# Kernel tuning notes

Hardware: AMD Instinct MI355X
Metric: run time of the kernel (lower is better)

Reference implementation:

```python
import jax, jax.numpy as jnp
import numpy as np

EPS = 1e-5

def mvn(x):
    # instance norm with torch's unbiased variance (ddof=1), eps added to var
    b, c = x.shape[:2]
    flat = x.reshape(b, c, -1)
    mean = flat.mean(axis=2)[:, :, None, None]
    std = jnp.sqrt(flat.var(axis=2, ddof=1) + EPS)[:, :, None, None]
    return (x - mean) / std

def conv1x1(x, w, b):
    # w: [Cout, Cin], b: [Cout], x: [B, Cin, H, W]
    return jnp.einsum('oc,bchw->bohw', w, x) + b[None, :, None, None]

def setup_inputs() -> dict:
    key = jax.random.key(0)
    ks = jax.random.split(key, 20)
    B, C, H, W = 4, 512, 64, 64
    s = 1.0 / np.sqrt(C)  # kaiming-ish scale for stable softmax logits
    inp = {
        'content': jax.random.normal(ks[0], (B, C, H, W), jnp.float32),
        'style':   jax.random.normal(ks[1], (B, C, H, W), jnp.float32),
        'v_w':   jax.random.normal(ks[2], (C, C), jnp.float32) * s,
        'v_b':   jax.random.normal(ks[3], (C,), jnp.float32) * 0.01,
        'vsp_w': jax.random.normal(ks[4], (1, C), jnp.float32) * s,
        'vsp_b': jax.random.normal(ks[5], (1,), jnp.float32) * 0.01,
        'k_w':   jax.random.normal(ks[6], (C, C), jnp.float32) * s,
        'k_b':   jax.random.normal(ks[7], (C,), jnp.float32) * 0.01,
        'qg_w':  jax.random.normal(ks[8], (C, C), jnp.float32) * s,
        'qg_b':  jax.random.normal(ks[9], (C,), jnp.float32) * 0.01,
        'g1_w1': jax.random.normal(ks[10], (C, C), jnp.float32) * s,
        'g1_b1': jax.random.normal(ks[11], (C,), jnp.float32) * 0.01,
        'g1_w2': jax.random.normal(ks[12], (C, C), jnp.float32) * s,
        'g1_b2': jax.random.normal(ks[13], (C,), jnp.float32) * 0.01,
        'g2_w1': jax.random.normal(ks[14], (C, C), jnp.float32) * s,
        'g2_b1': jax.random.normal(ks[15], (C,), jnp.float32) * 0.01,
        'g2_w2': jax.random.normal(ks[16], (C, C), jnp.float32) * s,
        'g2_b2': jax.random.normal(ks[17], (C,), jnp.float32) * 0.01,
    }
    return inp

def reference(content, style, v_w, v_b, vsp_w, vsp_b, k_w, k_b, qg_w, qg_b,
              g1_w1, g1_b1, g1_w2, g1_b2, g2_w1, g2_b1, g2_w2, g2_b2):
    b, c, h_s, w_s = style.shape
    _, _, h_c, w_c = content.shape
    Ls, Lc = h_s * w_s, h_c * w_c

    V = conv1x1(style, v_w, v_b)                                  # [b,c,hs,ws]
    key_pool = conv1x1(mvn(style), vsp_w, vsp_b).reshape(b, 1, Ls)
    style_weights = jax.nn.softmax(key_pool, axis=-1)             # [b,1,Ls]
    # global style vector: V_flat @ weights^T -> [b,c,1]
    gsv = jnp.einsum('bcl,bl->bc', V.reshape(b, c, Ls), style_weights[:, 0, :])
    gsv4 = gsv[:, :, None, None]                                  # [b,c,1,1]

    Q_guide = conv1x1(mvn(content), qg_w, qg_b)                   # [b,c,hc,wc]
    gamma = conv1x1(jax.nn.relu(conv1x1(gsv4, g1_w1, g1_b1)), g1_w2, g1_b2)
    beta  = conv1x1(jax.nn.relu(conv1x1(gsv4, g2_w1, g2_b1)), g2_w2, g2_b2)
    local_guidance = gamma * Q_guide + beta                       # [b,c,hc,wc]

    Q = (Q_guide + local_guidance).reshape(b, c, Lc).transpose(0, 2, 1)  # [b,Lc,c]
    K = conv1x1(style, k_w, k_b).reshape(b, c, Ls)                       # [b,c,Ls]
    vv = V.reshape(b, c, Ls).transpose(0, 2, 1)                          # [b,Ls,c]

    energy = jnp.einsum('bqc,bck->bqk', Q, K)                     # [b,Lc,Ls]
    S = jax.nn.softmax(energy, axis=-1)
    out = jnp.einsum('bqk,bkc->bqc', S, vv)                       # [b,Lc,c]
    out = out.transpose(0, 2, 1).reshape(b, c, h_c, w_c)
    return mvn(content) + out
```

## Files before the change

kernel.cpp:

```cpp
#include <hip/hip_runtime.h>
#include <math.h>

typedef __bf16 bf16_t;
typedef _Float16 f16_t;
typedef __attribute__((ext_vector_type(8))) __bf16 bf16x8;
typedef __attribute__((ext_vector_type(8))) _Float16 f16x8;
typedef __attribute__((ext_vector_type(4))) float f32x4;

namespace {
constexpr int Bn = 4;
constexpr int Cn = 512;
constexpr int Ln = 4096;
constexpr float kEps = 1e-5f;
constexpr size_t NQK = (size_t)Bn * Ln * Cn;
constexpr size_t CC  = (size_t)Cn * Cn;

constexpr size_t FOFF_MEANS = 0;
constexpr size_t FOFF_RSTDS = 2048;
constexpr size_t FOFF_MEANC = 4096;
constexpr size_t FOFF_RSTDC = 6144;
constexpr size_t FOFF_KP    = 8192;
constexpr size_t FOFF_GSV   = FOFF_KP + 16384;
constexpr size_t FOFF_H1    = FOFF_GSV + 2048;
constexpr size_t FOFF_H2    = FOFF_H1 + 2048;
constexpr size_t FOFF_GAMMA = FOFF_H2 + 2048;
constexpr size_t FOFF_BETA  = FOFF_GAMMA + 2048;
}

__device__ inline f32x4 mfma_bf(bf16x8 a, bf16x8 b, f32x4 c) {
    return __builtin_amdgcn_mfma_f32_16x16x32_bf16(a, b, c, 0, 0, 0);
}
__device__ inline f32x4 mfma_f16(f16x8 a, f16x8 b, f32x4 c) {
    return __builtin_amdgcn_mfma_f32_16x16x32_f16(a, b, c, 0, 0, 0);
}

__device__ __forceinline__ void gll16(const void* g, void* l) {
    __builtin_amdgcn_global_load_lds((const unsigned int*)g, (unsigned int*)l, 16, 0, 0);
}

__device__ inline unsigned short h2u(f16_t x) {
    union { f16_t h; unsigned short u; } c; c.h = x; return c.u;
}
__device__ inline f16_t u2h(unsigned short x) {
    union { f16_t h; unsigned short u; } c; c.u = x; return c.h;
}

__global__ __launch_bounds__(256) void stats_kernel(const float* __restrict__ x,
                                                    float* __restrict__ mean,
                                                    float* __restrict__ rstd) {
    int bc = blockIdx.x;
    const float* row = x + (size_t)bc * Ln;
    float s1 = 0.f, s2 = 0.f;
    for (int i = threadIdx.x; i < Ln; i += 256) {
        float v = row[i];
        s1 += v; s2 += v * v;
    }
    for (int off = 32; off; off >>= 1) {
        s1 += __shfl_down(s1, off);
        s2 += __shfl_down(s2, off);
    }
    __shared__ float a1[4], a2[4];
    int wid = threadIdx.x >> 6;
    if ((threadIdx.x & 63) == 0) { a1[wid] = s1; a2[wid] = s2; }
    __syncthreads();
    if (threadIdx.x == 0) {
        s1 = a1[0] + a1[1] + a1[2] + a1[3];
        s2 = a2[0] + a2[1] + a2[2] + a2[3];
        float m = s1 / Ln;
        float var = (s2 - m * s1) / (Ln - 1);
        mean[bc] = m;
        rstd[bc] = 1.0f / sqrtf(var + kEps);
    }
}

__global__ __launch_bounds__(256) void split_w_kernel(const float* __restrict__ w0,
                                                      const float* __restrict__ w1,
                                                      const float* __restrict__ w2,
                                                      bf16_t* __restrict__ wsp) {
    const float* w = (blockIdx.y == 0) ? w0 : (blockIdx.y == 1) ? w1 : w2;
    bf16_t* hi = wsp + (size_t)blockIdx.y * 2 * CC;
    bf16_t* lo = hi + CC;
    size_t i0 = ((size_t)blockIdx.x * 256 + threadIdx.x) * 8;
    float4 a = *(const float4*)(w + i0);
    float4 b = *(const float4*)(w + i0 + 4);
    float vs[8] = {a.x, a.y, a.z, a.w, b.x, b.y, b.z, b.w};
    bf16x8 hv, lv;
#pragma unroll
    for (int i = 0; i < 8; i++) {
        bf16_t h = (bf16_t)vs[i];
        hv[i] = h;
        lv[i] = (bf16_t)(vs[i] - (float)h);
    }
    *(bf16x8*)(hi + i0) = hv;
    *(bf16x8*)(lo + i0) = lv;
}

template <bool MVN>
__global__ __launch_bounds__(256) void split_xt_kernel(const float* __restrict__ x,
                                                       const float* __restrict__ mean,
                                                       const float* __restrict__ rstd,
                                                       bf16_t* __restrict__ hi,
                                                       bf16_t* __restrict__ lo) {
    __shared__ bf16_t th[32][40];
    __shared__ bf16_t tl[32][40];
    int b = blockIdx.z, c0 = blockIdx.y * 32, l0 = blockIdx.x * 32;
    const size_t base = (size_t)b * Cn * Ln;
    int lc = threadIdx.x & 31;
    int cr0 = threadIdx.x >> 5;
#pragma unroll
    for (int p = 0; p < 4; p++) {
        int cr = cr0 + p * 8;
        float v = x[base + (size_t)(c0 + cr) * Ln + l0 + lc];
        if constexpr (MVN) {
            v = (v - mean[b * Cn + c0 + cr]) * rstd[b * Cn + c0 + cr];
        }
        bf16_t h = (bf16_t)v;
        th[lc][cr] = h;
        tl[lc][cr] = (bf16_t)(v - (float)h);
    }
    __syncthreads();
    int tt = threadIdx.x & 127;
    int lrow = tt >> 2;
    int c8 = (tt & 3) * 8;
    if (threadIdx.x < 128) {
        *(bf16x8*)(hi + base + (size_t)(l0 + lrow) * Cn + c0 + c8) = *(bf16x8*)&th[lrow][c8];
    } else {
        *(bf16x8*)(lo + base + (size_t)(l0 + lrow) * Cn + c0 + c8) = *(bf16x8*)&tl[lrow][c8];
    }
}

template <int MODE>
__global__ __launch_bounds__(256, 2) void conv_mfma_kernel(
    const bf16_t* __restrict__ Whi, const bf16_t* __restrict__ Wlo,
    const bf16_t* __restrict__ Xhi, const bf16_t* __restrict__ Xlo,
    const float* __restrict__ bias,
    const float* __restrict__ gma, const float* __restrict__ bta,
    f16_t* __restrict__ out0) {
    const int b = blockIdx.z;
    const int o0 = blockIdx.y * 128;
    const int l0 = blockIdx.x * 128;
    const int tid = threadIdx.x;
    const int lane = tid & 63, wid = tid >> 6;
    const int wm = wid & 1, wn = wid >> 1;
    const int lg = lane >> 4, li = lane & 15;
    const size_t bLC = (size_t)b * Ln * Cn;

    __shared__ __align__(16) char smem[66560];

    f32x4 acc[4][4];
#pragma unroll
    for (int i = 0; i < 4; i++)
#pragma unroll
        for (int j = 0; j < 4; j++) acc[i][j] = (f32x4){0.f, 0.f, 0.f, 0.f};

    for (int cc = 0; cc < Cn; cc += 64) {
        __syncthreads();
#pragma unroll
        for (int p = 0; p < 4; p++) {
            int idx = p * 256 + tid;
            int row = idx >> 3;
            int c8 = (idx & 7) * 8;
            unsigned off = (unsigned)((row * 64 + c8) * 2) ^ (unsigned)((row & 7) << 4);
            *(bf16x8*)(smem + off)         = *(const bf16x8*)(Whi + (size_t)(o0 + row) * Cn + cc + c8);
            *(bf16x8*)(smem + 16384 + off) = *(const bf16x8*)(Wlo + (size_t)(o0 + row) * Cn + cc + c8);
            *(bf16x8*)(smem + 32768 + off) = *(const bf16x8*)(Xhi + bLC + (size_t)(l0 + row) * Cn + cc + c8);
            *(bf16x8*)(smem + 49152 + off) = *(const bf16x8*)(Xlo + bLC + (size_t)(l0 + row) * Cn + cc + c8);
        }
        __syncthreads();
#pragma unroll
        for (int k2 = 0; k2 < 2; k2++) {
            bf16x8 ah[4], al[4], bh[4], bl[4];
#pragma unroll
            for (int f = 0; f < 4; f++) {
                int row = wm * 64 + f * 16 + li;
                unsigned ob = (unsigned)(row * 128 + ((k2 * 64 + lg * 16) ^ ((row & 7) << 4)));
                ah[f] = *(const bf16x8*)(smem + ob);
                al[f] = *(const bf16x8*)(smem + 16384 + ob);
            }
#pragma unroll
            for (int f = 0; f < 4; f++) {
                int row = wn * 64 + f * 16 + li;
                unsigned ob = (unsigned)(row * 128 + ((k2 * 64 + lg * 16) ^ ((row & 7) << 4)));
                bh[f] = *(const bf16x8*)(smem + 32768 + ob);
                bl[f] = *(const bf16x8*)(smem + 49152 + ob);
            }
#pragma unroll
            for (int fm = 0; fm < 4; fm++)
#pragma unroll
                for (int fn = 0; fn < 4; fn++) {
                    acc[fm][fn] = mfma_bf(ah[fm], bh[fn], acc[fm][fn]);
                    acc[fm][fn] = mfma_bf(ah[fm], bl[fn], acc[fm][fn]);
                    acc[fm][fn] = mfma_bf(al[fm], bh[fn], acc[fm][fn]);
                }
        }
    }

    if constexpr (MODE == 0) {
        const size_t bCL = (size_t)b * Cn * Ln;
#pragma unroll
        for (int fm = 0; fm < 4; fm++) {
#pragma unroll
            for (int r = 0; r < 4; r++) {
                int o = o0 + wm * 64 + fm * 16 + lg * 4 + r;
                float bv = bias[o];
#pragma unroll
                for (int fn = 0; fn < 4; fn++) {
                    int l = l0 + wn * 64 + fn * 16 + li;
                    out0[bCL + (size_t)o * Ln + l] = (f16_t)(acc[fm][fn][r] + bv);
                }
            }
        }
    } else {
        __syncthreads();
        unsigned short* ep = (unsigned short*)smem;
#pragma unroll
        for (int fm = 0; fm < 4; fm++) {
#pragma unroll
            for (int r = 0; r < 4; r++) {
                int orow = wm * 64 + fm * 16 + lg * 4 + r;
                int o = o0 + orow;
                float bv = bias[o];
                float gv = 0.f, btv = 0.f;
                if constexpr (MODE == 2) { gv = gma[b * Cn + o]; btv = bta[b * Cn + o]; }
#pragma unroll
                for (int fn = 0; fn < 4; fn++) {
                    int lrow = wn * 64 + fn * 16 + li;
                    float v = acc[fm][fn][r] + bv;
                    if constexpr (MODE == 2) v = v * (1.f + gv) + btv;
                    ep[lrow * 130 + orow] = h2u((f16_t)v);
                }
            }
        }
        __syncthreads();
#pragma unroll
        for (int p = 0; p < 8; p++) {
            int idx = p * 256 + tid;
            int lrow = idx >> 4;
            int c8 = (idx & 15) * 8;
            f16x8 hv;
#pragma unroll
            for (int u = 0; u < 8; u++) hv[u] = u2h(ep[lrow * 130 + c8 + u]);
            *(f16x8*)(out0 + bLC + (size_t)(l0 + lrow) * Cn + o0 + c8) = hv;
        }
    }
}

__global__ __launch_bounds__(256) void keypool_kernel(const float* __restrict__ style,
                                                      const float* __restrict__ vsp_w,
                                                      const float* __restrict__ vsp_b,
                                                      const float* __restrict__ mean_s,
                                                      const float* __restrict__ rstd_s,
                                                      float* __restrict__ kp) {
    int b = blockIdx.y;
    int l = blockIdx.x * 256 + threadIdx.x;
    const size_t bCL = (size_t)b * Cn * Ln;
    float acc = 0.f;
    for (int c = 0; c < Cn; c++) {
        float v = style[bCL + (size_t)c * Ln + l];
        acc += vsp_w[c] * (v - mean_s[b * Cn + c]) * rstd_s[b * Cn + c];
    }
    kp[b * Ln + l] = acc + vsp_b[0];
}

__global__ __launch_bounds__(1024) void softmax_kp_kernel(float* __restrict__ kp) {
    int b = blockIdx.x;
    float* p = kp + (size_t)b * Ln;
    int tid = threadIdx.x;
    float v[4];
    float m = -3e38f;
#pragma unroll
    for (int j = 0; j < 4; j++) { v[j] = p[tid + 1024 * j]; m = fmaxf(m, v[j]); }
    __shared__ float red[16];
    for (int off = 32; off; off >>= 1) m = fmaxf(m, __shfl_down(m, off));
    if ((tid & 63) == 0) red[tid >> 6] = m;
    __syncthreads();
    if (tid == 0) {
        float mm = red[0];
        for (int i = 1; i < 16; i++) mm = fmaxf(mm, red[i]);
        red[0] = mm;
    }
    __syncthreads();
    m = red[0];
    __syncthreads();
    float e[4]; float s = 0.f;
#pragma unroll
    for (int j = 0; j < 4; j++) { e[j] = __expf(v[j] - m); s += e[j]; }
    for (int off = 32; off; off >>= 1) s += __shfl_down(s, off);
    if ((tid & 63) == 0) red[tid >> 6] = s;
    __syncthreads();
    if (tid == 0) {
        float ss = 0.f;
        for (int i = 0; i < 16; i++) ss += red[i];
        red[0] = ss;
    }
    __syncthreads();
    float inv = 1.0f / red[0];
#pragma unroll
    for (int j = 0; j < 4; j++) p[tid + 1024 * j] = e[j] * inv;
}

__global__ __launch_bounds__(256) void gsv_kernel(const f16_t* __restrict__ Vf,
                                                  const float* __restrict__ w,
                                                  float* __restrict__ gsv) {
    int c = blockIdx.x, b = blockIdx.y;
    int tid = threadIdx.x;
    const f16_t* vp = Vf + ((size_t)b * Cn + c) * Ln;
    const float* wp = w + (size_t)b * Ln;
    float acc = 0.f;
    for (int base = tid * 8; base < Ln; base += 2048) {
        f16x8 v = *(const f16x8*)(vp + base);
        float4 w0 = *(const float4*)(wp + base);
        float4 w1 = *(const float4*)(wp + base + 4);
        acc += (float)v[0] * w0.x + (float)v[1] * w0.y + (float)v[2] * w0.z + (float)v[3] * w0.w;
        acc += (float)v[4] * w1.x + (float)v[5] * w1.y + (float)v[6] * w1.z + (float)v[7] * w1.w;
    }
    for (int off = 32; off; off >>= 1) acc += __shfl_down(acc, off);
    __shared__ float red[4];
    if ((tid & 63) == 0) red[tid >> 6] = acc;
    __syncthreads();
    if (tid == 0) gsv[(size_t)b * Cn + c] = red[0] + red[1] + red[2] + red[3];
}

__global__ __launch_bounds__(256) void mlp_hidden_kernel(const float* __restrict__ gsv,
                                                         const float* __restrict__ w1a, const float* __restrict__ b1a,
                                                         const float* __restrict__ w1b, const float* __restrict__ b1b,
                                                         float* __restrict__ h1, float* __restrict__ h2) {
    int idx = blockIdx.x * 256 + threadIdx.x;
    int b = idx / Cn, c = idx % Cn;
    float a1 = b1a[c], a2 = b1b[c];
    for (int k = 0; k < Cn; k++) {
        float g = gsv[b * Cn + k];
        a1 += w1a[(size_t)c * Cn + k] * g;
        a2 += w1b[(size_t)c * Cn + k] * g;
    }
    h1[idx] = fmaxf(a1, 0.f);
    h2[idx] = fmaxf(a2, 0.f);
}

__global__ __launch_bounds__(256) void mlp_out_kernel(const float* __restrict__ h1, const float* __restrict__ h2,
                                                      const float* __restrict__ w2a, const float* __restrict__ b2a,
                                                      const float* __restrict__ w2b, const float* __restrict__ b2b,
                                                      float* __restrict__ gamma, float* __restrict__ beta) {
    int idx = blockIdx.x * 256 + threadIdx.x;
    int b = idx / Cn, c = idx % Cn;
    float a1 = b2a[c], a2 = b2b[c];
    for (int k = 0; k < Cn; k++) {
        a1 += w2a[(size_t)c * Cn + k] * h1[b * Cn + k];
        a2 += w2b[(size_t)c * Cn + k] * h2[b * Cn + k];
    }
    gamma[idx] = a1;
    beta[idx] = a2;
}

__global__ __launch_bounds__(256, 2) void flash_kernel(
    const f16_t* __restrict__ Qf, const f16_t* __restrict__ Kf,
    const f16_t* __restrict__ Vf, float* __restrict__ Ot) {
    const int b = blockIdx.y;
    const int q0 = blockIdx.x * 32;
    const int tid = threadIdx.x;
    const int lane = tid & 63;
    const int wn = tid >> 6;
    const int lg = lane >> 4, li = lane & 15;

    __shared__ __align__(16) f16_t q_s[32 * 512];
    __shared__ __align__(16) f16_t pb_s[32 * 64];
    __shared__ float smx[4][32];
    __shared__ float sml[4][32];

    const size_t qbase = ((size_t)b * Ln + q0) * Cn;
    const size_t kbase = (size_t)b * Ln * Cn;
    const size_t vbase = (size_t)b * Cn * Ln;

#pragma unroll
    for (int i = 0; i < 8; i++) {
        int idx = i * 256 + tid;
        int row = idx >> 6, slot = idx & 63;
        int sp = (slot & 56) | ((slot & 7) ^ (row & 7));
        gll16(Qf + qbase + (size_t)row * Cn + sp * 8, q_s + (size_t)idx * 8);
    }
    __syncthreads();

    const int key = wn * 16 + li;

    f16x8 kreg[2][2];
    auto loadK = [&](int g, int slot) {
        int ktA = (g >> 3) << 6;
        int cc = (g & 7) * 64;
        const f16_t* kp = Kf + kbase + (size_t)(ktA + key) * Cn + cc + lg * 8;
        kreg[slot][0] = *(const f16x8*)(kp);
        kreg[slot][1] = *(const f16x8*)(kp + 32);
    };
    loadK(0, 0);
    loadK(1, 1);

    f32x4 o[2][8];
#pragma unroll
    for (int m = 0; m < 2; m++)
#pragma unroll
        for (int j = 0; j < 8; j++) o[m][j] = (f32x4){0.f, 0.f, 0.f, 0.f};
    float m_run[2][4], l_run[2][4];
#pragma unroll
    for (int m = 0; m < 2; m++)
#pragma unroll
        for (int r = 0; r < 4; r++) { m_run[m][r] = -1e30f; l_run[m][r] = 0.f; }

    for (int tile = 0; tile < 64; tile++) {
        const int kt = tile * 64;
        f32x4 e[2];
#pragma unroll
        for (int m = 0; m < 2; m++) e[m] = (f32x4){0.f, 0.f, 0.f, 0.f};

#pragma unroll
        for (int cs = 0; cs < 8; cs++) {
            const int slot = cs & 1;
            f16x8 k0 = kreg[slot][0], k1 = kreg[slot][1];
            {
                int g2 = (tile * 8 + cs + 2) & 511;
                loadK(g2, slot);
            }
            f16x8 aq0[2], aq1[2];
#pragma unroll
            for (int m = 0; m < 2; m++) {
                int row = m * 16 + li;
                unsigned swz = (unsigned)((row & 7) << 4);
                aq0[m] = *(const f16x8*)((const char*)q_s + row * 1024 + ((cs * 128 + lg * 16) ^ swz));
                aq1[m] = *(const f16x8*)((const char*)q_s + row * 1024 + ((cs * 128 + 64 + lg * 16) ^ swz));
            }
            __builtin_amdgcn_s_setprio(1);
#pragma unroll
            for (int m = 0; m < 2; m++) {
                e[m] = mfma_f16(aq0[m], k0, e[m]);
                e[m] = mfma_f16(aq1[m], k1, e[m]);
            }
            __builtin_amdgcn_s_setprio(0);
        }

        f16x8 va[2], vb[2];
        {
            const f16_t* vp0 = Vf + vbase + (size_t)(wn * 16 + li) * Ln + kt + lg * 8;
            va[0] = *(const f16x8*)(vp0);
            vb[0] = *(const f16x8*)(vp0 + 32);
            const f16_t* vp1 = Vf + vbase + (size_t)((4 + wn) * 16 + li) * Ln + kt + lg * 8;
            va[1] = *(const f16x8*)(vp1);
            vb[1] = *(const f16x8*)(vp1 + 32);
        }

        float tmax[2][4];
#pragma unroll
        for (int m = 0; m < 2; m++)
#pragma unroll
            for (int r = 0; r < 4; r++) tmax[m][r] = e[m][r];
#pragma unroll
        for (int d = 1; d < 16; d <<= 1)
#pragma unroll
            for (int m = 0; m < 2; m++)
#pragma unroll
                for (int r = 0; r < 4; r++) tmax[m][r] = fmaxf(tmax[m][r], __shfl_xor(tmax[m][r], d));
        if (li == 0) {
#pragma unroll
            for (int m = 0; m < 2; m++)
#pragma unroll
                for (int r = 0; r < 4; r++) smx[wn][m * 16 + lg * 4 + r] = tmax[m][r];
        }
        asm volatile("s_waitcnt lgkmcnt(0)\n\ts_barrier" ::: "memory");
        float scv[2][4];
        bool anyresc = false;
#pragma unroll
        for (int m = 0; m < 2; m++)
#pragma unroll
            for (int r = 0; r < 4; r++) {
                int row = m * 16 + lg * 4 + r;
                float tm = fmaxf(fmaxf(smx[0][row], smx[1][row]), fmaxf(smx[2][row], smx[3][row]));
                float mnew = fmaxf(m_run[m][r], tm);
                scv[m][r] = __expf(m_run[m][r] - mnew);
                anyresc |= (mnew > m_run[m][r]);
                m_run[m][r] = mnew;
            }
        float pv[2][4], rsum[2][4];
#pragma unroll
        for (int m = 0; m < 2; m++)
#pragma unroll
            for (int r = 0; r < 4; r++) {
                float pe = __expf(e[m][r] - m_run[m][r]);
                pv[m][r] = pe;
                rsum[m][r] = pe;
            }
#pragma unroll
        for (int d = 1; d < 16; d <<= 1)
#pragma unroll
            for (int m = 0; m < 2; m++)
#pragma unroll
                for (int r = 0; r < 4; r++) rsum[m][r] += __shfl_xor(rsum[m][r], d);
        if (li == 0) {
#pragma unroll
            for (int m = 0; m < 2; m++)
#pragma unroll
                for (int r = 0; r < 4; r++) sml[wn][m * 16 + lg * 4 + r] = rsum[m][r];
        }
#pragma unroll
        for (int m = 0; m < 2; m++)
#pragma unroll
            for (int r = 0; r < 4; r++) {
                int qrow = m * 16 + lg * 4 + r;
                unsigned boff = (unsigned)(qrow * 128 + ((2 * key) ^ ((qrow & 7) << 4)));
                *(f16_t*)((char*)pb_s + boff) = (f16_t)pv[m][r];
            }
        if (__any((int)anyresc)) {
#pragma unroll
            for (int m = 0; m < 2; m++)
#pragma unroll
                for (int j = 0; j < 8; j++)
#pragma unroll
                    for (int r = 0; r < 4; r++) o[m][j][r] *= scv[m][r];
        }
        asm volatile("s_waitcnt lgkmcnt(0)\n\ts_barrier" ::: "memory");
#pragma unroll
        for (int m = 0; m < 2; m++)
#pragma unroll
            for (int r = 0; r < 4; r++) {
                int row = m * 16 + lg * 4 + r;
                l_run[m][r] = l_run[m][r] * scv[m][r] + sml[0][row] + sml[1][row] + sml[2][row] + sml[3][row];
            }

        f16x8 pa[2][2];
#pragma unroll
        for (int m = 0; m < 2; m++)
#pragma unroll
            for (int k2 = 0; k2 < 2; k2++) {
                int qrow = m * 16 + li;
                pa[m][k2] = *(const f16x8*)((const char*)pb_s + qrow * 128 +
                              ((k2 * 64 + lg * 16) ^ ((qrow & 7) << 4)));
            }
#pragma unroll
        for (int n = 0; n < 8; n++) {
            const int slot = n & 1;
            f16x8 c0 = va[slot], c1 = vb[slot];
            if (n + 2 < 8) {
                int cg = (n + 2) * 4 + wn;
                const f16_t* vp = Vf + vbase + (size_t)(cg * 16 + li) * Ln + kt + lg * 8;
                va[slot] = *(const f16x8*)(vp);
                vb[slot] = *(const f16x8*)(vp + 32);
            }
            __builtin_amdgcn_s_setprio(1);
#pragma unroll
            for (int m = 0; m < 2; m++) {
                o[m][n] = mfma_f16(pa[m][0], c0, o[m][n]);
                o[m][n] = mfma_f16(pa[m][1], c1, o[m][n]);
            }
            __builtin_amdgcn_s_setprio(0);
        }
    }

#pragma unroll
    for (int m = 0; m < 2; m++)
#pragma unroll
        for (int r = 0; r < 4; r++) l_run[m][r] = 1.f / l_run[m][r];
#pragma unroll
    for (int m = 0; m < 2; m++)
#pragma unroll
        for (int n = 0; n < 8; n++) {
            int c = (n * 4 + wn) * 16 + li;
            int qg = q0 + m * 16 + lg * 4;
            float4 ov;
            ov.x = o[m][n][0] * l_run[m][0];
            ov.y = o[m][n][1] * l_run[m][1];
            ov.z = o[m][n][2] * l_run[m][2];
            ov.w = o[m][n][3] * l_run[m][3];
            *(float4*)(Ot + vbase + (size_t)c * Ln + qg) = ov;
        }
}

__global__ __launch_bounds__(256) void final_kernel(const float* __restrict__ content,
                                                    const float* __restrict__ mean_c,
                                                    const float* __restrict__ rstd_c,
                                                    float* __restrict__ out) {
    size_t gid = (size_t)blockIdx.x * 256 + threadIdx.x;
    size_t linear = gid * 4;
    int ch = (int)(linear / Ln);
    float m = mean_c[ch], rs = rstd_c[ch];
    float4 cv = *(const float4*)(content + linear);
    float4 ov = *(const float4*)(out + linear);
    ov.x += (cv.x - m) * rs;
    ov.y += (cv.y - m) * rs;
    ov.z += (cv.z - m) * rs;
    ov.w += (cv.w - m) * rs;
    *(float4*)(out + linear) = ov;
}

extern "C" void kernel_launch(void* const* d_in, const int* in_sizes, int n_in,
                              void* d_out, int out_size, void* d_ws, size_t ws_size,
                              hipStream_t stream) {
    const float* content = (const float*)d_in[0];
    const float* style   = (const float*)d_in[1];
    const float* v_w   = (const float*)d_in[2];
    const float* v_b   = (const float*)d_in[3];
    const float* vsp_w = (const float*)d_in[4];
    const float* vsp_b = (const float*)d_in[5];
    const float* k_w   = (const float*)d_in[6];
    const float* k_b   = (const float*)d_in[7];
    const float* qg_w  = (const float*)d_in[8];
    const float* qg_b  = (const float*)d_in[9];
    const float* g1_w1 = (const float*)d_in[10];
    const float* g1_b1 = (const float*)d_in[11];
    const float* g1_w2 = (const float*)d_in[12];
    const float* g1_b2 = (const float*)d_in[13];
    const float* g2_w1 = (const float*)d_in[14];
    const float* g2_b1 = (const float*)d_in[15];
    const float* g2_w2 = (const float*)d_in[16];
    const float* g2_b2 = (const float*)d_in[17];

    f16_t* wsh = (f16_t*)d_ws;
    f16_t* Qf = wsh;
    f16_t* Kf = wsh + NQK;
    f16_t* Vf = wsh + 2 * NQK;
    bf16_t* wsp = (bf16_t*)(wsh + 3 * NQK);
    bf16_t* Wv_hi = wsp;            bf16_t* Wv_lo = wsp + CC;
    bf16_t* Wk_hi = wsp + 2 * CC;   bf16_t* Wk_lo = wsp + 3 * CC;
    bf16_t* Wq_hi = wsp + 4 * CC;   bf16_t* Wq_lo = wsp + 5 * CC;

    float* wsf = (float*)(wsp + 6 * CC);
    float* mean_s = wsf + FOFF_MEANS;
    float* rstd_s = wsf + FOFF_RSTDS;
    float* mean_c = wsf + FOFF_MEANC;
    float* rstd_c = wsf + FOFF_RSTDC;
    float* kp     = wsf + FOFF_KP;
    float* gsv    = wsf + FOFF_GSV;
    float* h1     = wsf + FOFF_H1;
    float* h2     = wsf + FOFF_H2;
    float* gamma  = wsf + FOFF_GAMMA;
    float* beta   = wsf + FOFF_BETA;

    bf16_t* XThi = (bf16_t*)d_out;
    bf16_t* XTlo = XThi + NQK;
    float* outF  = (float*)d_out;

    stats_kernel<<<dim3(Bn * Cn), 256, 0, stream>>>(style, mean_s, rstd_s);
    stats_kernel<<<dim3(Bn * Cn), 256, 0, stream>>>(content, mean_c, rstd_c);

    split_w_kernel<<<dim3(CC / 2048, 3), 256, 0, stream>>>(v_w, k_w, qg_w, wsp);
    split_xt_kernel<false><<<dim3(Ln / 32, Cn / 32, Bn), 256, 0, stream>>>(style, nullptr, nullptr, XThi, XTlo);

    dim3 cgrid(Ln / 128, Cn / 128, Bn);
    conv_mfma_kernel<0><<<cgrid, 256, 0, stream>>>(Wv_hi, Wv_lo, XThi, XTlo, v_b, nullptr, nullptr, Vf);

    keypool_kernel<<<dim3(Ln / 256, Bn), 256, 0, stream>>>(style, vsp_w, vsp_b, mean_s, rstd_s, kp);
    softmax_kp_kernel<<<dim3(Bn), 1024, 0, stream>>>(kp);
    gsv_kernel<<<dim3(Cn, Bn), 256, 0, stream>>>(Vf, kp, gsv);
    mlp_hidden_kernel<<<dim3(Bn * Cn / 256), 256, 0, stream>>>(gsv, g1_w1, g1_b1, g2_w1, g2_b1, h1, h2);
    mlp_out_kernel<<<dim3(Bn * Cn / 256), 256, 0, stream>>>(h1, h2, g1_w2, g1_b2, g2_w2, g2_b2, gamma, beta);

    conv_mfma_kernel<1><<<cgrid, 256, 0, stream>>>(Wk_hi, Wk_lo, XThi, XTlo, k_b, nullptr, nullptr, Kf);

    split_xt_kernel<true><<<dim3(Ln / 32, Cn / 32, Bn), 256, 0, stream>>>(content, mean_c, rstd_c, XThi, XTlo);
    conv_mfma_kernel<2><<<cgrid, 256, 0, stream>>>(Wq_hi, Wq_lo, XThi, XTlo, qg_b, gamma, beta, Qf);

    flash_kernel<<<dim3(Ln / 32, Bn), 256, 0, stream>>>(Qf, Kf, Vf, outF);

    final_kernel<<<dim3((Bn * Cn * (Ln / 4)) / 256), 256, 0, stream>>>(content, mean_c, rstd_c, outF);
}
```

Measured before the change: 709.0 us.

## Halve flash query tile to 16 rows and remap blocks across XCDs

Each flash-attention workgroup now handles 16 query rows instead of 32, doubling the grid to 1024 blocks. A 1D grid with an XCD-aware remap (bid&7)*128+(bid>>3) groups blocks of the same batch on the same chiplet, aiming for better L2 reuse of K/V. The QK accumulation is split into two independent MFMA chains to increase ILP. The trade-off is that K and V are re-read from memory twice as often per query, and fewer MFMAs are issued per load and per barrier.

After: 1.145 ms. 1.61x slower.

```diff
diff --git a/kernel.cpp b/kernel.cpp
--- a/kernel.cpp
+++ b/kernel.cpp
@@ -355,24 +355,27 @@
 __global__ __launch_bounds__(256, 2) void flash_kernel(
     const f16_t* __restrict__ Qf, const f16_t* __restrict__ Kf,
     const f16_t* __restrict__ Vf, float* __restrict__ Ot) {
-    const int b = blockIdx.y;
-    const int q0 = blockIdx.x * 32;
+    const int bid = blockIdx.x;
+    const int wgid = (bid & 7) * 128 + (bid >> 3);
+    const int b = wgid >> 8;
+    const int q0 = (wgid & 255) * 16;
+
     const int tid = threadIdx.x;
     const int lane = tid & 63;
     const int wn = tid >> 6;
     const int lg = lane >> 4, li = lane & 15;
 
-    __shared__ __align__(16) f16_t q_s[32 * 512];
-    __shared__ __align__(16) f16_t pb_s[32 * 64];
-    __shared__ float smx[4][32];
-    __shared__ float sml[4][32];
+    __shared__ __align__(16) f16_t q_s[16 * 512];
+    __shared__ __align__(16) f16_t pb_s[16 * 64];
+    __shared__ float smx[4][16];
+    __shared__ float sml[4][16];
 
     const size_t qbase = ((size_t)b * Ln + q0) * Cn;
     const size_t kbase = (size_t)b * Ln * Cn;
     const size_t vbase = (size_t)b * Cn * Ln;
 
 #pragma unroll
-    for (int i = 0; i < 8; i++) {
+    for (int i = 0; i < 4; i++) {
         int idx = i * 256 + tid;
         int row = idx >> 6, slot = idx & 63;
         int sp = (slot & 56) | ((slot & 7) ^ (row & 7));
@@ -393,22 +396,17 @@
     loadK(0, 0);
     loadK(1, 1);
 
-    f32x4 o[2][8];
-#pragma unroll
-    for (int m = 0; m < 2; m++)
-#pragma unroll
-        for (int j = 0; j < 8; j++) o[m][j] = (f32x4){0.f, 0.f, 0.f, 0.f};
-    float m_run[2][4], l_run[2][4];
-#pragma unroll
-    for (int m = 0; m < 2; m++)
-#pragma unroll
-        for (int r = 0; r < 4; r++) { m_run[m][r] = -1e30f; l_run[m][r] = 0.f; }
+    f32x4 o[8];
+#pragma unroll
+    for (int j = 0; j < 8; j++) o[j] = (f32x4){0.f, 0.f, 0.f, 0.f};
+    float m_run[4], l_run[4];
+#pragma unroll
+    for (int r = 0; r < 4; r++) { m_run[r] = -1e30f; l_run[r] = 0.f; }
 
     for (int tile = 0; tile < 64; tile++) {
         const int kt = tile * 64;
-        f32x4 e[2];
-#pragma unroll
-        for (int m = 0; m < 2; m++) e[m] = (f32x4){0.f, 0.f, 0.f, 0.f};
+        f32x4 eA = (f32x4){0.f, 0.f, 0.f, 0.f};
+        f32x4 eB = (f32x4){0.f, 0.f, 0.f, 0.f};
 
 #pragma unroll
         for (int cs = 0; cs < 8; cs++) {
@@ -418,22 +416,18 @@
                 int g2 = (tile * 8 + cs + 2) & 511;
                 loadK(g2, slot);
             }
-            f16x8 aq0[2], aq1[2];
-#pragma unroll
-            for (int m = 0; m < 2; m++) {
-                int row = m * 16 + li;
-                unsigned swz = (unsigned)((row & 7) << 4);
-                aq0[m] = *(const f16x8*)((const char*)q_s + row * 1024 + ((cs * 128 + lg * 16) ^ swz));
-                aq1[m] = *(const f16x8*)((const char*)q_s + row * 1024 + ((cs * 128 + 64 + lg * 16) ^ swz));
-            }
+            int row = li;
+            unsigned swz = (unsigned)((row & 7) << 4);
+            f16x8 aq0 = *(const f16x8*)((const char*)q_s + row * 1024 + ((cs * 128 + lg * 16) ^ swz));
+            f16x8 aq1 = *(const f16x8*)((const char*)q_s + row * 1024 + ((cs * 128 + 64 + lg * 16) ^ swz));
             __builtin_amdgcn_s_setprio(1);
-#pragma unroll
-            for (int m = 0; m < 2; m++) {
-                e[m] = mfma_f16(aq0[m], k0, e[m]);
-                e[m] = mfma_f16(aq1[m], k1, e[m]);
-            }
+            eA = mfma_f16(aq0, k0, eA);
+            eB = mfma_f16(aq1, k1, eB);
             __builtin_amdgcn_s_setprio(0);
         }
+        f32x4 e;
+#pragma unroll
+        for (int r = 0; r < 4; r++) e[r] = eA[r] + eB[r];
 
         f16x8 va[2], vb[2];
         {
@@ -445,92 +439,70 @@
             vb[1] = *(const f16x8*)(vp1 + 32);
         }
 
-        float tmax[2][4];
-#pragma unroll
-        for (int m = 0; m < 2; m++)
-#pragma unroll
-            for (int r = 0; r < 4; r++) tmax[m][r] = e[m][r];
+        float tmax[4];
+#pragma unroll
+        for (int r = 0; r < 4; r++) tmax[r] = e[r];
 #pragma unroll
         for (int d = 1; d < 16; d <<= 1)
 #pragma unroll
-            for (int m = 0; m < 2; m++)
-#pragma unroll
-                for (int r = 0; r < 4; r++) tmax[m][r] = fmaxf(tmax[m][r], __shfl_xor(tmax[m][r], d));
+            for (int r = 0; r < 4; r++) tmax[r] = fmaxf(tmax[r], __shfl_xor(tmax[r], d));
         if (li == 0) {
 #pragma unroll
-            for (int m = 0; m < 2; m++)
-#pragma unroll
-                for (int r = 0; r < 4; r++) smx[wn][m * 16 + lg * 4 + r] = tmax[m][r];
+            for (int r = 0; r < 4; r++) smx[wn][lg * 4 + r] = tmax[r];
         }
         asm volatile("s_waitcnt lgkmcnt(0)\n\ts_barrier" ::: "memory");
-        float scv[2][4];
+        float scv[4];
         bool anyresc = false;
 #pragma unroll
-        for (int m = 0; m < 2; m++)
-#pragma unroll
-            for (int r = 0; r < 4; r++) {
-                int row = m * 16 + lg * 4 + r;
-                float tm = fmaxf(fmaxf(smx[0][row], smx[1][row]), fmaxf(smx[2][row], smx[3][row]));
-                float mnew = fmaxf(m_run[m][r], tm);
-                scv[m][r] = __expf(m_run[m][r] - mnew);
-                anyresc |= (mnew > m_run[m][r]);
-                m_run[m][r] = mnew;
-            }
-        float pv[2][4], rsum[2][4];
-#pragma unroll
-        for (int m = 0; m < 2; m++)
-#pragma unroll
-            for (int r = 0; r < 4; r++) {
-                float pe = __expf(e[m][r] - m_run[m][r]);
-                pv[m][r] = pe;
-                rsum[m][r] = pe;
-            }
+        for (int r = 0; r < 4; r++) {
+            int row = lg * 4 + r;
+            float tm = fmaxf(fmaxf(smx[0][row], smx[1][row]), fmaxf(smx[2][row], smx[3][row]));
+            float mnew = fmaxf(m_run[r], tm);
+            scv[r] = __expf(m_run[r] - mnew);
+            anyresc |= (mnew > m_run[r]);
+            m_run[r] = mnew;
+        }
+        float pv[4], rsum[4];
+#pragma unroll
+        for (int r = 0; r < 4; r++) {
+            float pe = __expf(e[r] - m_run[r]);
+            pv[r] = pe;
+            rsum[r] = pe;
+        }
 #pragma unroll
         for (int d = 1; d < 16; d <<= 1)
 #pragma unroll
-            for (int m = 0; m < 2; m++)
-#pragma unroll
-                for (int r = 0; r < 4; r++) rsum[m][r] += __shfl_xor(rsum[m][r], d);
+            for (int r = 0; r < 4; r++) rsum[r] += __shfl_xor(rsum[r], d);
         if (li == 0) {
 #pragma unroll
-            for (int m = 0; m < 2; m++)
-#pragma unroll
-                for (int r = 0; r < 4; r++) sml[wn][m * 16 + lg * 4 + r] = rsum[m][r];
-        }
-#pragma unroll
-        for (int m = 0; m < 2; m++)
-#pragma unroll
-            for (int r = 0; r < 4; r++) {
-                int qrow = m * 16 + lg * 4 + r;
-                unsigned boff = (unsigned)(qrow * 128 + ((2 * key) ^ ((qrow & 7) << 4)));
-                *(f16_t*)((char*)pb_s + boff) = (f16_t)pv[m][r];
-            }
+            for (int r = 0; r < 4; r++) sml[wn][lg * 4 + r] = rsum[r];
+        }
+#pragma unroll
+        for (int r = 0; r < 4; r++) {
+            int qrow = lg * 4 + r;
+            unsigned boff = (unsigned)(qrow * 128 + ((2 * key) ^ ((qrow & 7) << 4)));
+            *(f16_t*)((char*)pb_s + boff) = (f16_t)pv[r];
+        }
         if (__any((int)anyresc)) {
 #pragma unroll
-            for (int m = 0; m < 2; m++)
-#pragma unroll
-                for (int j = 0; j < 8; j++)
-#pragma unroll
-                    for (int r = 0; r < 4; r++) o[m][j][r] *= scv[m][r];
+            for (int j = 0; j < 8; j++)
+#pragma unroll
+                for (int r = 0; r < 4; r++) o[j][r] *= scv[r];
         }
         asm volatile("s_waitcnt lgkmcnt(0)\n\ts_barrier" ::: "memory");
 #pragma unroll
-        for (int m = 0; m < 2; m++)
-#pragma unroll
-            for (int r = 0; r < 4; r++) {
-                int row = m * 16 + lg * 4 + r;
-                l_run[m][r] = l_run[m][r] * scv[m][r] + sml[0][row] + sml[1][row] + sml[2][row] + sml[3][row];
-            }
-
-        f16x8 pa[2][2];
-#pragma unroll
-        for (int m = 0; m < 2; m++)
-#pragma unroll
-            for (int k2 = 0; k2 < 2; k2++) {
-                int qrow = m * 16 + li;
-                pa[m][k2] = *(const f16x8*)((const char*)pb_s + qrow * 128 +
-                              ((k2 * 64 + lg * 16) ^ ((qrow & 7) << 4)));
-            }
+        for (int r = 0; r < 4; r++) {
+            int row = lg * 4 + r;
+            l_run[r] = l_run[r] * scv[r] + sml[0][row] + sml[1][row] + sml[2][row] + sml[3][row];
+        }
+
+        f16x8 pa[2];
+#pragma unroll
+        for (int k2 = 0; k2 < 2; k2++) {
+            int qrow = li;
+            pa[k2] = *(const f16x8*)((const char*)pb_s + qrow * 128 +
+                          ((k2 * 64 + lg * 16) ^ ((qrow & 7) << 4)));
+        }
 #pragma unroll
         for (int n = 0; n < 8; n++) {
             const int slot = n & 1;
@@ -542,32 +514,25 @@
                 vb[slot] = *(const f16x8*)(vp + 32);
             }
             __builtin_amdgcn_s_setprio(1);
-#pragma unroll
-            for (int m = 0; m < 2; m++) {
-                o[m][n] = mfma_f16(pa[m][0], c0, o[m][n]);
-                o[m][n] = mfma_f16(pa[m][1], c1, o[m][n]);
-            }
+            o[n] = mfma_f16(pa[0], c0, o[n]);
+            o[n] = mfma_f16(pa[1], c1, o[n]);
             __builtin_amdgcn_s_setprio(0);
         }
     }
 
 #pragma unroll
-    for (int m = 0; m < 2; m++)
-#pragma unroll
-        for (int r = 0; r < 4; r++) l_run[m][r] = 1.f / l_run[m][r];
-#pragma unroll
-    for (int m = 0; m < 2; m++)
-#pragma unroll
-        for (int n = 0; n < 8; n++) {
-            int c = (n * 4 + wn) * 16 + li;
-            int qg = q0 + m * 16 + lg * 4;
-            float4 ov;
-            ov.x = o[m][n][0] * l_run[m][0];
-            ov.y = o[m][n][1] * l_run[m][1];
-            ov.z = o[m][n][2] * l_run[m][2];
-            ov.w = o[m][n][3] * l_run[m][3];
-            *(float4*)(Ot + vbase + (size_t)c * Ln + qg) = ov;
-        }
+    for (int r = 0; r < 4; r++) l_run[r] = 1.f / l_run[r];
+#pragma unroll
+    for (int n = 0; n < 8; n++) {
+        int c = (n * 4 + wn) * 16 + li;
+        int qg = q0 + lg * 4;
+        float4 ov;
+        ov.x = o[n][0] * l_run[0];
+        ov.y = o[n][1] * l_run[1];
+        ov.z = o[n][2] * l_run[2];
+        ov.w = o[n][3] * l_run[3];
+        *(float4*)(Ot + vbase + (size_t)c * Ln + qg) = ov;
+    }
 }
 
 __global__ __launch_bounds__(256) void final_kernel(const float* __restrict__ content,
@@ -654,7 +619,7 @@
     split_xt_kernel<true><<<dim3(Ln / 32, Cn / 32, Bn), 256, 0, stream>>>(content, mean_c, rstd_c, XThi, XTlo);
     conv_mfma_kernel<2><<<cgrid, 256, 0, stream>>>(Wq_hi, Wq_lo, XThi, XTlo, qg_b, gamma, beta, Qf);
 
-    flash_kernel<<<dim3(Ln / 32, Bn), 256, 0, stream>>>(Qf, Kf, Vf, outF);
+    flash_kernel<<<dim3((Ln / 16) * Bn), 256, 0, stream>>>(Qf, Kf, Vf, outF);
 
     final_kernel<<<dim3((Bn * Cn * (Ln / 4)) / 256), 256, 0, stream>>>(content, mean_c, rstd_c, outF);
 }
```

## Enlarge flash tile to 64 queries with 8 waves and LDS-staged K ring

Applied to the files above, without the earlier changes.

The flash attention kernel now handles 64 query rows per workgroup with 512 threads instead of 32 rows with 256 threads. K tiles are staged into a triple-buffered shared-memory ring with async global-to-LDS loads, replacing per-wave register prefetch, so each K tile is fetched once per block and reused across more queries. Running max, sum and rescale state move into shared per-row arrays, and workgroup IDs are remapped for locality. The cost is more LDS (about 100KB), an extra barrier per channel step and per tile, and fewer blocks per CU, which may limit occupancy.

Result: no change. 715.5 us (+0.9%).

```diff
diff --git a/kernel.cpp b/kernel.cpp
--- a/kernel.cpp
+++ b/kernel.cpp
@@ -352,20 +352,28 @@
     beta[idx] = a2;
 }
 
-__global__ __launch_bounds__(256, 2) void flash_kernel(
+__global__ __launch_bounds__(512, 2) void flash_kernel(
     const f16_t* __restrict__ Qf, const f16_t* __restrict__ Kf,
     const f16_t* __restrict__ Vf, float* __restrict__ Ot) {
-    const int b = blockIdx.y;
-    const int q0 = blockIdx.x * 32;
+    const int bid = blockIdx.x;
+    const int wgid = (bid & 7) * 32 + (bid >> 3);
+    const int b = wgid >> 6;
+    const int q0 = (wgid & 63) * 64;
+
     const int tid = threadIdx.x;
     const int lane = tid & 63;
-    const int wn = tid >> 6;
+    const int wid = tid >> 6;
+    const int wm = wid & 1;
+    const int wn = wid >> 1;
     const int lg = lane >> 4, li = lane & 15;
 
-    __shared__ __align__(16) f16_t q_s[32 * 512];
-    __shared__ __align__(16) f16_t pb_s[32 * 64];
-    __shared__ float smx[4][32];
-    __shared__ float sml[4][32];
+    __shared__ __align__(16) f16_t q_s[64 * 512];
+    __shared__ __align__(16) f16_t kbuf[3 * 4096];
+    __shared__ __align__(16) f16_t pb_s[64 * 64];
+    __shared__ float smx[4][64];
+    __shared__ float sml[4][64];
+    __shared__ float mrow[64], lrow[64], srow[64];
+    __shared__ int rflag;
 
     const size_t qbase = ((size_t)b * Ln + q0) * Cn;
     const size_t kbase = (size_t)b * Ln * Cn;
@@ -373,74 +381,85 @@
 
 #pragma unroll
     for (int i = 0; i < 8; i++) {
-        int idx = i * 256 + tid;
+        int idx = i * 512 + tid;
         int row = idx >> 6, slot = idx & 63;
         int sp = (slot & 56) | ((slot & 7) ^ (row & 7));
         gll16(Qf + qbase + (size_t)row * Cn + sp * 8, q_s + (size_t)idx * 8);
     }
+
+    const int skey = tid >> 3;
+    const int ssp  = ((tid & 7) ^ (skey & 7)) * 8;
+    auto stageK = [&](int g, int ring) {
+        int ktA = (g >> 3) << 6;
+        int cc  = (g & 7) * 64;
+        gll16(Kf + kbase + (size_t)(ktA + skey) * Cn + cc + ssp,
+              kbuf + (size_t)ring * 4096 + (size_t)tid * 8);
+    };
+    stageK(0, 0);
+    stageK(1, 1);
+
+    if (tid < 64) { mrow[tid] = -1e30f; lrow[tid] = 0.f; srow[tid] = 1.f; }
+    if (tid == 0) rflag = 0;
     __syncthreads();
 
     const int key = wn * 16 + li;
-
-    f16x8 kreg[2][2];
-    auto loadK = [&](int g, int slot) {
-        int ktA = (g >> 3) << 6;
-        int cc = (g & 7) * 64;
-        const f16_t* kp = Kf + kbase + (size_t)(ktA + key) * Cn + cc + lg * 8;
-        kreg[slot][0] = *(const f16x8*)(kp);
-        kreg[slot][1] = *(const f16x8*)(kp + 32);
-    };
-    loadK(0, 0);
-    loadK(1, 1);
-
-    f32x4 o[2][8];
-#pragma unroll
-    for (int m = 0; m < 2; m++)
-#pragma unroll
-        for (int j = 0; j < 8; j++) o[m][j] = (f32x4){0.f, 0.f, 0.f, 0.f};
-    float m_run[2][4], l_run[2][4];
-#pragma unroll
-    for (int m = 0; m < 2; m++)
-#pragma unroll
-        for (int r = 0; r < 4; r++) { m_run[m][r] = -1e30f; l_run[m][r] = 0.f; }
+    const unsigned kswz = (unsigned)((key & 7) << 4);
+    const unsigned kfoff0 = (unsigned)(key * 128 + ((lg * 16) ^ kswz));
+    const unsigned kfoff1 = (unsigned)(key * 128 + ((64 + lg * 16) ^ kswz));
+    const int cbase = wid * 64;
+
+    f32x4 o[4][4];
+#pragma unroll
+    for (int m2 = 0; m2 < 4; m2++)
+#pragma unroll
+        for (int n = 0; n < 4; n++) o[m2][n] = (f32x4){0.f, 0.f, 0.f, 0.f};
 
     for (int tile = 0; tile < 64; tile++) {
         const int kt = tile * 64;
         f32x4 e[2];
-#pragma unroll
-        for (int m = 0; m < 2; m++) e[m] = (f32x4){0.f, 0.f, 0.f, 0.f};
+        e[0] = (f32x4){0.f, 0.f, 0.f, 0.f};
+        e[1] = (f32x4){0.f, 0.f, 0.f, 0.f};
 
 #pragma unroll
         for (int cs = 0; cs < 8; cs++) {
-            const int slot = cs & 1;
-            f16x8 k0 = kreg[slot][0], k1 = kreg[slot][1];
+            const int cur = tile * 8 + cs;
+            if (cs == 7) {
+                if (tile == 63) { asm volatile("s_waitcnt vmcnt(0)" ::: "memory"); }
+                else            { asm volatile("s_waitcnt vmcnt(1)" ::: "memory"); }
+            } else {
+                asm volatile("s_waitcnt vmcnt(1)" ::: "memory");
+            }
+            asm volatile("s_barrier" ::: "memory");
             {
-                int g2 = (tile * 8 + cs + 2) & 511;
-                loadK(g2, slot);
-            }
-            f16x8 aq0[2], aq1[2];
+                int c2 = cur + 2;
+                if (c2 < 512) stageK(c2, c2 % 3);
+            }
+            const char* kb = (const char*)kbuf + (size_t)(cur % 3) * 8192;
+            f16x8 bk0 = *(const f16x8*)(kb + kfoff0);
+            f16x8 bk1 = *(const f16x8*)(kb + kfoff1);
+            f16x8 qa0[2], qa1[2];
 #pragma unroll
             for (int m = 0; m < 2; m++) {
-                int row = m * 16 + li;
+                int row = wm * 32 + m * 16 + li;
                 unsigned swz = (unsigned)((row & 7) << 4);
-                aq0[m] = *(const f16x8*)((const char*)q_s + row * 1024 + ((cs * 128 + lg * 16) ^ swz));
-                aq1[m] = *(const f16x8*)((const char*)q_s + row * 1024 + ((cs * 128 + 64 + lg * 16) ^ swz));
+                qa0[m] = *(const f16x8*)((const char*)q_s + row * 1024 + ((cs * 128 + lg * 16) ^ swz));
+                qa1[m] = *(const f16x8*)((const char*)q_s + row * 1024 + ((cs * 128 + 64 + lg * 16) ^ swz));
             }
             __builtin_amdgcn_s_setprio(1);
 #pragma unroll
             for (int m = 0; m < 2; m++) {
-                e[m] = mfma_f16(aq0[m], k0, e[m]);
-                e[m] = mfma_f16(aq1[m], k1, e[m]);
+                e[m] = mfma_f16(qa0[m], bk0, e[m]);
+                e[m] = mfma_f16(qa1[m], bk1, e[m]);
             }
             __builtin_amdgcn_s_setprio(0);
         }
 
         f16x8 va[2], vb[2];
         {
-            const f16_t* vp0 = Vf + vbase + (size_t)(wn * 16 + li) * Ln + kt + lg * 8;
+            const f16_t* vp0 = Vf + vbase + (size_t)(cbase + li) * Ln + kt + lg * 8;
             va[0] = *(const f16x8*)(vp0);
             vb[0] = *(const f16x8*)(vp0 + 32);
-            const f16_t* vp1 = Vf + vbase + (size_t)((4 + wn) * 16 + li) * Ln + kt + lg * 8;
+            const f16_t* vp1 = Vf + vbase + (size_t)(cbase + 16 + li) * Ln + kt + lg * 8;
             va[1] = *(const f16x8*)(vp1);
             vb[1] = *(const f16x8*)(vp1 + 32);
         }
@@ -460,29 +479,27 @@
 #pragma unroll
             for (int m = 0; m < 2; m++)
 #pragma unroll
-                for (int r = 0; r < 4; r++) smx[wn][m * 16 + lg * 4 + r] = tmax[m][r];
-        }
+                for (int r = 0; r < 4; r++) smx[wn][wm * 32 + m * 16 + lg * 4 + r] = tmax[m][r];
+        }
+        if (tid == 0) rflag = 0;
         asm volatile("s_waitcnt lgkmcnt(0)\n\ts_barrier" ::: "memory");
-        float scv[2][4];
-        bool anyresc = false;
+        if (tid < 64) {
+            float mold = mrow[tid];
+            float tm = fmaxf(fmaxf(smx[0][tid], smx[1][tid]), fmaxf(smx[2][tid], smx[3][tid]));
+            float mnew = fmaxf(mold, tm);
+            srow[tid] = __expf(mold - mnew);
+            mrow[tid] = mnew;
+            if (mnew > mold) rflag = 1;
+        }
+        asm volatile("s_waitcnt lgkmcnt(0)\n\ts_barrier" ::: "memory");
+        float pvv[2][4], rsum[2][4];
 #pragma unroll
         for (int m = 0; m < 2; m++)
 #pragma unroll
             for (int r = 0; r < 4; r++) {
-                int row = m * 16 + lg * 4 + r;
-                float tm = fmaxf(fmaxf(smx[0][row], smx[1][row]), fmaxf(smx[2][row], smx[3][row]));
-                float mnew = fmaxf(m_run[m][r], tm);
-                scv[m][r] = __expf(m_run[m][r] - mnew);
-                anyresc |= (mnew > m_run[m][r]);
-                m_run[m][r] = mnew;
-            }
-        float pv[2][4], rsum[2][4];
-#pragma unroll
-        for (int m = 0; m < 2; m++)
-#pragma unroll
-            for (int r = 0; r < 4; r++) {
-                float pe = __expf(e[m][r] - m_run[m][r]);
-                pv[m][r] = pe;
+                int row = wm * 32 + m * 16 + lg * 4 + r;
+                float pe = __expf(e[m][r] - mrow[row]);
+                pvv[m][r] = pe;
                 rsum[m][r] = pe;
             }
 #pragma unroll
@@ -495,79 +512,76 @@
 #pragma unroll
             for (int m = 0; m < 2; m++)
 #pragma unroll
-                for (int r = 0; r < 4; r++) sml[wn][m * 16 + lg * 4 + r] = rsum[m][r];
+                for (int r = 0; r < 4; r++) sml[wn][wm * 32 + m * 16 + lg * 4 + r] = rsum[m][r];
         }
 #pragma unroll
         for (int m = 0; m < 2; m++)
 #pragma unroll
             for (int r = 0; r < 4; r++) {
-                int qrow = m * 16 + lg * 4 + r;
-                unsigned boff = (unsigned)(qrow * 128 + ((2 * key) ^ ((qrow & 7) << 4)));
-                *(f16_t*)((char*)pb_s + boff) = (f16_t)pv[m][r];
-            }
-        if (__any((int)anyresc)) {
-#pragma unroll
-            for (int m = 0; m < 2; m++)
-#pragma unroll
-                for (int j = 0; j < 8; j++)
-#pragma unroll
-                    for (int r = 0; r < 4; r++) o[m][j][r] *= scv[m][r];
-        }
+                int row = wm * 32 + m * 16 + lg * 4 + r;
+                unsigned boff = (unsigned)(row * 128 + ((2 * key) ^ ((row & 7) << 4)));
+                *(f16_t*)((char*)pb_s + boff) = (f16_t)pvv[m][r];
+            }
         asm volatile("s_waitcnt lgkmcnt(0)\n\ts_barrier" ::: "memory");
-#pragma unroll
-        for (int m = 0; m < 2; m++)
-#pragma unroll
-            for (int r = 0; r < 4; r++) {
-                int row = m * 16 + lg * 4 + r;
-                l_run[m][r] = l_run[m][r] * scv[m][r] + sml[0][row] + sml[1][row] + sml[2][row] + sml[3][row];
-            }
-
-        f16x8 pa[2][2];
-#pragma unroll
-        for (int m = 0; m < 2; m++)
+        if (tid < 64)
+            lrow[tid] = lrow[tid] * srow[tid] + sml[0][tid] + sml[1][tid] + sml[2][tid] + sml[3][tid];
+
+        f16x8 pa[4][2];
+#pragma unroll
+        for (int m2 = 0; m2 < 4; m2++)
 #pragma unroll
             for (int k2 = 0; k2 < 2; k2++) {
-                int qrow = m * 16 + li;
-                pa[m][k2] = *(const f16x8*)((const char*)pb_s + qrow * 128 +
-                              ((k2 * 64 + lg * 16) ^ ((qrow & 7) << 4)));
-            }
-#pragma unroll
-        for (int n = 0; n < 8; n++) {
+                int row = m2 * 16 + li;
+                pa[m2][k2] = *(const f16x8*)((const char*)pb_s + row * 128 +
+                              ((k2 * 64 + lg * 16) ^ ((row & 7) << 4)));
+            }
+        if (rflag) {
+#pragma unroll
+            for (int m2 = 0; m2 < 4; m2++)
+#pragma unroll
+                for (int r = 0; r < 4; r++) {
+                    float s = srow[m2 * 16 + lg * 4 + r];
+#pragma unroll
+                    for (int n = 0; n < 4; n++) o[m2][n][r] *= s;
+                }
+        }
+#pragma unroll
+        for (int n = 0; n < 4; n++) {
             const int slot = n & 1;
             f16x8 c0 = va[slot], c1 = vb[slot];
-            if (n + 2 < 8) {
-                int cg = (n + 2) * 4 + wn;
-                const f16_t* vp = Vf + vbase + (size_t)(cg * 16 + li) * Ln + kt + lg * 8;
+            if (n < 2) {
+                const f16_t* vp = Vf + vbase + (size_t)(cbase + (n + 2) * 16 + li) * Ln + kt + lg * 8;
                 va[slot] = *(const f16x8*)(vp);
                 vb[slot] = *(const f16x8*)(vp + 32);
             }
             __builtin_amdgcn_s_setprio(1);
 #pragma unroll
-            for (int m = 0; m < 2; m++) {
-                o[m][n] = mfma_f16(pa[m][0], c0, o[m][n]);
-                o[m][n] = mfma_f16(pa[m][1], c1, o[m][n]);
+            for (int m2 = 0; m2 < 4; m2++) {
+                o[m2][n] = mfma_f16(pa[m2][0], c0, o[m2][n]);
+                o[m2][n] = mfma_f16(pa[m2][1], c1, o[m2][n]);
             }
             __builtin_amdgcn_s_setprio(0);
         }
     }
 
-#pragma unroll
-    for (int m = 0; m < 2; m++)
-#pragma unroll
-        for (int r = 0; r < 4; r++) l_run[m][r] = 1.f / l_run[m][r];
-#pragma unroll
-    for (int m = 0; m < 2; m++)
-#pragma unroll
-        for (int n = 0; n < 8; n++) {
-            int c = (n * 4 + wn) * 16 + li;
-            int qg = q0 + m * 16 + lg * 4;
+    __syncthreads();
+#pragma unroll
+    for (int m2 = 0; m2 < 4; m2++) {
+        float lv[4];
+#pragma unroll
+        for (int r = 0; r < 4; r++) lv[r] = 1.f / lrow[m2 * 16 + lg * 4 + r];
+#pragma unroll
+        for (int n = 0; n < 4; n++) {
+            int c = cbase + n * 16 + li;
+            int qg = q0 + m2 * 16 + lg * 4;
             float4 ov;
-            ov.x = o[m][n][0] * l_run[m][0];
-            ov.y = o[m][n][1] * l_run[m][1];
-            ov.z = o[m][n][2] * l_run[m][2];
-            ov.w = o[m][n][3] * l_run[m][3];
+            ov.x = o[m2][n][0] * lv[0];
+            ov.y = o[m2][n][1] * lv[1];
+            ov.z = o[m2][n][2] * lv[2];
+            ov.w = o[m2][n][3] * lv[3];
             *(float4*)(Ot + vbase + (size_t)c * Ln + qg) = ov;
         }
+    }
 }
 
 __global__ __launch_bounds__(256) void final_kernel(const float* __restrict__ content,
@@ -654,7 +668,7 @@
     split_xt_kernel<true><<<dim3(Ln / 32, Cn / 32, Bn), 256, 0, stream>>>(content, mean_c, rstd_c, XThi, XTlo);
     conv_mfma_kernel<2><<<cgrid, 256, 0, stream>>>(Wq_hi, Wq_lo, XThi, XTlo, qg_b, gamma, beta, Qf);
 
-    flash_kernel<<<dim3(Ln / 32, Bn), 256, 0, stream>>>(Qf, Kf, Vf, outF);
+    flash_kernel<<<dim3((Ln / 64) * Bn), 512, 0, stream>>>(Qf, Kf, Vf, outF);
 
     final_kernel<<<dim3((Bn * Cn * (Ln / 4)) / 256), 256, 0, stream>>>(content, mean_c, rstd_c, outF);
 }
```
